# Kernel optimization log

Measured on AMD Instinct MI355X. Metric: run time of the kernel, lower is better.

## Reference

```python
import jax, jax.numpy as jnp
import numpy as np

# hyperparameters from init_kwargs
TEMP = 0.05
MOMENTUM = 0.2
ALPHA = 0.9
TEMP_DIST = 0.6
LAMBDA1 = 1.0
LAMBDA2 = 1.0
EPS_CONS = 2.0
NUM_SAMPLES = 8192
NUM_FEATURES = 2048
B = 256
K = 20
EPS = 1e-12


def setup_inputs() -> dict:
    key = jax.random.key(0)
    ks = jax.random.split(key, 8)
    inputs0 = jax.random.normal(ks[0], (B, NUM_FEATURES), dtype=jnp.float32)
    logits0 = jax.random.normal(ks[1], (B, NUM_SAMPLES), dtype=jnp.float32)
    logits1 = jax.random.normal(ks[2], (B, NUM_SAMPLES), dtype=jnp.float32)
    targets = jax.random.randint(ks[3], (B,), 0, NUM_SAMPLES, dtype=jnp.int32)
    indexes = jnp.arange(B, dtype=jnp.int32)  # global idx == batch idx (identity idx2bidx)
    neighbors = jax.random.randint(ks[4], (B, K), 0, B, dtype=jnp.int32)
    neighbor_dists = jax.random.uniform(ks[5], (B, K), dtype=jnp.float32)
    rampup = jnp.ones((), dtype=jnp.float32)
    features = jax.random.normal(ks[6], (NUM_SAMPLES, NUM_FEATURES), dtype=jnp.float32)
    features = features / jnp.linalg.norm(features, axis=1, keepdims=True)
    return {
        'inputs0': inputs0, 'logits0': logits0, 'logits1': logits1,
        'targets': targets, 'indexes': indexes, 'neighbors': neighbors,
        'neighbor_dists': neighbor_dists, 'rampup': rampup, 'features': features,
    }


def reference(inputs0, logits0, logits1, targets, indexes, neighbors,
              neighbor_dists, rampup, features):
    # F.normalize(inputs[0], dim=1)
    x = inputs0 / jnp.maximum(jnp.linalg.norm(inputs0, axis=1, keepdims=True), EPS)

    # CM forward: scores against memory bank, scaled by temperature
    outputs = (x @ features.T) / TEMP                      # [B, S]
    logp = jax.nn.log_softmax(outputs, axis=-1)
    loss_nce = -jnp.mean(jnp.take_along_axis(logp, targets[:, None], axis=1))

    targets_onehot = jax.nn.one_hot(targets, NUM_SAMPLES, dtype=logits0.dtype)

    # neighbor gathering: indexes = arange(B) so idx2bidx is identity; every
    # neighbor in [0,B) passes the `nb in indexes` filter.
    p0 = jax.nn.softmax(logits0, axis=-1)[neighbors]       # [B, K, S]
    p1 = jax.nn.softmax(logits1, axis=-1)[neighbors]       # [B, K, S]
    # loop appends logits0-row then logits1-row per neighbor -> interleave
    p = jnp.stack([p0, p1], axis=2).reshape(B, 2 * K, NUM_SAMPLES)
    d2 = jnp.repeat(neighbor_dists, 2, axis=1)             # [B, 2K] (d,d pairs)
    w = jax.nn.softmax(d2 / TEMP_DIST, axis=1)             # [B, 2K]
    logits_neighbors1 = jnp.einsum('bk,bks->bs', w, p)     # [B, S]

    # KL branch: neighbors with dist <= eps_consistency (all, since eps=2.0)
    mask = (neighbor_dists <= EPS_CONS).astype(p0.dtype)   # [B, K]
    cnt = jnp.maximum(mask.sum(axis=1, keepdims=True), 1.0)
    logits_neighbors1_KL = jnp.einsum('bk,bks->bs', mask, p0) / cnt  # [B, S]

    refined = ALPHA * targets_onehot + (1.0 - ALPHA) * jax.lax.stop_gradient(logits_neighbors1)
    loss_ce = jnp.mean(jnp.sum(-refined * jax.nn.log_softmax(logits0, axis=-1), axis=1))

    # KLDivLoss(logsoftmax(logits1).detach(), target) with batchmean reduction
    lp1 = jax.lax.stop_gradient(jax.nn.log_softmax(logits1, axis=-1))
    t = logits_neighbors1_KL
    kl = jnp.sum(jnp.where(t > 0, t * (jnp.log(jnp.maximum(t, EPS)) - lp1), 0.0)) / B

    # CM momentum memory-bank scatter update (backward side-effect in torch);
    # equivalent to the sequential loop when targets are unique in the batch.
    upd = MOMENTUM * features[targets] + (1.0 - MOMENTUM) * x
    upd = upd / jnp.maximum(jnp.linalg.norm(upd, axis=1, keepdims=True), EPS)
    new_features = features.at[targets].set(upd)

    return (loss_nce, LAMBDA1 * loss_ce, LAMBDA2 * rampup * kl, new_features)
```

## Files before the change

kernel.cpp:

```cpp
#include <hip/hip_runtime.h>
#include <cmath>

#define NB 256
#define NS 8192
#define NF 2048
#define NK 20

typedef _Float16 half8 __attribute__((ext_vector_type(8)));
typedef _Float16 half4 __attribute__((ext_vector_type(4)));
typedef float f32x4 __attribute__((ext_vector_type(4)));

__device__ __forceinline__ void async16(const void* g, void* l) {
  __builtin_amdgcn_global_load_lds(
      (const __attribute__((address_space(1))) unsigned int*)g,
      (__attribute__((address_space(3))) unsigned int*)l, 16, 0, 0);
}

__device__ __forceinline__ float waveSum(float v) {
#pragma unroll
  for (int off = 32; off > 0; off >>= 1) v += __shfl_xor(v, off, 64);
  return v;
}
__device__ __forceinline__ float waveMax(float v) {
#pragma unroll
  for (int off = 32; off > 0; off >>= 1) v = fmaxf(v, __shfl_xor(v, off, 64));
  return v;
}

__global__ __launch_bounds__(256, 1) void prep(
    const float4* __restrict__ f4, const float* __restrict__ in0,
    const float* __restrict__ logits0, const float* __restrict__ logits1,
    const int* __restrict__ targets, const int* __restrict__ neighbors,
    const float* __restrict__ ndist,
    float* __restrict__ outF, _Float16* __restrict__ fh,
    _Float16* __restrict__ Pt, _Float16* __restrict__ xh,
    _Float16* __restrict__ alpha_h, float* __restrict__ mll,
    _Float16* __restrict__ Wp, float* __restrict__ loss) {
  __shared__ alignas(16) union {
    struct {
      float redA[4];
      float redB[4];
      unsigned long long wmask[4];
    } s;
    _Float16 Lt[16 * 520];
  } sm;
  int tid = threadIdx.x, blk = blockIdx.x;
  int wave = tid >> 6, lane = tid & 63;

  if (blk < NS) {
    int row = blk;
    const float4* fr = f4 + (size_t)row * (NF / 4);
    float4 v0 = fr[tid], v1 = fr[tid + 256];
    half4 h0, h1;
    h0[0] = (_Float16)v0.x; h0[1] = (_Float16)v0.y; h0[2] = (_Float16)v0.z; h0[3] = (_Float16)v0.w;
    h1[0] = (_Float16)v1.x; h1[1] = (_Float16)v1.y; h1[2] = (_Float16)v1.z; h1[3] = (_Float16)v1.w;
    ((half4*)(fh + (size_t)row * NF))[tid] = h0;
    ((half4*)(fh + (size_t)row * NF))[tid + 256] = h1;
    unsigned long long mk = __ballot(targets[tid] == row);
    if (lane == 0) sm.s.wmask[wave] = mk;
    __syncthreads();
    int u = -1;
#pragma unroll
    for (int w = 3; w >= 0; --w)
      if (u < 0 && sm.s.wmask[w])
        u = w * 64 + 63 - (int)__clzll(sm.s.wmask[w]);
    if (u >= 0) {
      const float4* xr = (const float4*)(in0 + (size_t)u * NF);
      float4 a0 = xr[tid], a1 = xr[tid + 256];
      float ssx = a0.x * a0.x + a0.y * a0.y + a0.z * a0.z + a0.w * a0.w +
                  a1.x * a1.x + a1.y * a1.y + a1.z * a1.z + a1.w * a1.w;
      float w1 = waveSum(ssx);
      if (lane == 0) sm.s.redA[wave] = w1;
      __syncthreads();
      float totx = (sm.s.redA[0] + sm.s.redA[1]) + (sm.s.redA[2] + sm.s.redA[3]);
      float ix = 0.8f / fmaxf(sqrtf(totx), 1e-12f);
      v0 = make_float4(0.2f * v0.x + ix * a0.x, 0.2f * v0.y + ix * a0.y,
                       0.2f * v0.z + ix * a0.z, 0.2f * v0.w + ix * a0.w);
      v1 = make_float4(0.2f * v1.x + ix * a1.x, 0.2f * v1.y + ix * a1.y,
                       0.2f * v1.z + ix * a1.z, 0.2f * v1.w + ix * a1.w);
      float ss = v0.x * v0.x + v0.y * v0.y + v0.z * v0.z + v0.w * v0.w +
                 v1.x * v1.x + v1.y * v1.y + v1.z * v1.z + v1.w * v1.w;
      float w2 = waveSum(ss);
      if (lane == 0) sm.s.redB[wave] = w2;
      __syncthreads();
      float tot = (sm.s.redB[0] + sm.s.redB[1]) + (sm.s.redB[2] + sm.s.redB[3]);
      float inv = 1.0f / fmaxf(sqrtf(tot), 1e-12f);
      v0.x *= inv; v0.y *= inv; v0.z *= inv; v0.w *= inv;
      v1.x *= inv; v1.y *= inv; v1.z *= inv; v1.w *= inv;
    }
    float4* o4 = (float4*)(outF + (size_t)row * NF);
    o4[tid] = v0;
    o4[tid + 256] = v1;
  } else if (blk < NS + 512) {
    int r = blk - NS;
    const float* src = (r < NB) ? logits0 : logits1;
    const float4* row = (const float4*)(src + (size_t)(r & (NB - 1)) * NS);
    float4 v[8];
    float mx = -1e30f;
#pragma unroll
    for (int i = 0; i < 8; ++i) {
      v[i] = row[tid + i * 256];
      mx = fmaxf(mx, fmaxf(fmaxf(v[i].x, v[i].y), fmaxf(v[i].z, v[i].w)));
    }
    float wv = waveMax(mx);
    if (lane == 0) sm.s.redA[wave] = wv;
    __syncthreads();
    float m = fmaxf(fmaxf(sm.s.redA[0], sm.s.redA[1]), fmaxf(sm.s.redA[2], sm.s.redA[3]));
    float se = 0.0f;
#pragma unroll
    for (int i = 0; i < 8; ++i)
      se += expf(v[i].x - m) + expf(v[i].y - m) + expf(v[i].z - m) + expf(v[i].w - m);
    float sw = waveSum(se);
    if (lane == 0) sm.s.redB[wave] = sw;
    __syncthreads();
    float l = (sm.s.redB[0] + sm.s.redB[1]) + (sm.s.redB[2] + sm.s.redB[3]);
    if (tid == 0) {
      mll[r] = m + logf(l);
      alpha_h[r] = (_Float16)(256.0f * expf(-m) / l);
    }
  } else if (blk < NS + 1024) {
    int s0 = (blk - (NS + 512)) * 16;
#pragma unroll
    for (int g = 0; g < 8; ++g) {
      int pos = g * 256 + tid;
      int row = pos >> 2, c4 = pos & 3;
      const float* src = ((row < NB) ? logits0 + (size_t)row * NS
                                     : logits1 + (size_t)(row - NB) * NS) + s0 + c4 * 4;
      float4 v = *(const float4*)src;
      sm.Lt[(c4 * 4 + 0) * 520 + row] = (_Float16)expf(v.x);
      sm.Lt[(c4 * 4 + 1) * 520 + row] = (_Float16)expf(v.y);
      sm.Lt[(c4 * 4 + 2) * 520 + row] = (_Float16)expf(v.z);
      sm.Lt[(c4 * 4 + 3) * 520 + row] = (_Float16)expf(v.w);
    }
    __syncthreads();
    int srow = tid >> 4, seg = tid & 15;
    _Float16* dst = Pt + (size_t)(s0 + srow) * 512 + seg * 32;
    const _Float16* lsrc = &sm.Lt[srow * 520 + seg * 32];
#pragma unroll
    for (int q = 0; q < 4; ++q)
      *(half8*)(dst + q * 8) = *(const half8*)(lsrc + q * 8);
  } else if (blk < NS + 1280) {
    int b = blk - (NS + 1024);
    const float4* row = (const float4*)(in0 + (size_t)b * NF);
    float4 v0 = row[tid], v1 = row[tid + 256];
    float ss = v0.x * v0.x + v0.y * v0.y + v0.z * v0.z + v0.w * v0.w +
               v1.x * v1.x + v1.y * v1.y + v1.z * v1.z + v1.w * v1.w;
    float w = waveSum(ss);
    if (lane == 0) sm.s.redA[wave] = w;
    __syncthreads();
    float tot = (sm.s.redA[0] + sm.s.redA[1]) + (sm.s.redA[2] + sm.s.redA[3]);
    float inv = 1.0f / fmaxf(sqrtf(tot), 1e-12f);
    half4 h0, h1;
    h0[0] = (_Float16)(v0.x * inv); h0[1] = (_Float16)(v0.y * inv);
    h0[2] = (_Float16)(v0.z * inv); h0[3] = (_Float16)(v0.w * inv);
    h1[0] = (_Float16)(v1.x * inv); h1[1] = (_Float16)(v1.y * inv);
    h1[2] = (_Float16)(v1.z * inv); h1[3] = (_Float16)(v1.w * inv);
    ((half4*)(xh + (size_t)b * NF))[tid] = h0;
    ((half4*)(xh + (size_t)b * NF))[tid + 256] = h1;
  } else {
    if (tid < 3) loss[tid] = 0.0f;
    float4* W4 = (float4*)Wp;
    for (int i = tid; i < 512 * 512 * 2 / 16; i += 256) W4[i] = make_float4(0, 0, 0, 0);
    __syncthreads();
    int b = tid;
    float d[NK], e[NK];
    int n[NK];
    float s = 0.0f;
    int cnt = 0;
#pragma unroll
    for (int k = 0; k < NK; ++k) {
      d[k] = ndist[b * NK + k];
      n[k] = neighbors[b * NK + k];
      e[k] = expf(d[k] * (1.0f / 0.6f));
      s += e[k];
      cnt += (d[k] <= 2.0f) ? 1 : 0;
    }
    float invs = 1.0f / (2.0f * s);
    float invc = 1.0f / fmaxf((float)cnt, 1.0f);
    _Float16* rkl = Wp + (size_t)b * 512;
    _Float16* rce = Wp + (size_t)(256 + b) * 512;
#pragma unroll
    for (int k = 0; k < NK; ++k) {
      bool first = true;
#pragma unroll
      for (int k2 = 0; k2 < NK; ++k2)
        if (k2 < k && n[k2] == n[k]) first = false;
      if (first) {
        float wsum = 0.0f, ksum = 0.0f;
#pragma unroll
        for (int k2 = 0; k2 < NK; ++k2)
          if (k2 >= k && n[k2] == n[k]) {
            wsum += e[k2] * invs;
            ksum += (d[k2] <= 2.0f) ? invc : 0.0f;
          }
        rkl[n[k]] = (_Float16)ksum;
        rce[n[k]] = (_Float16)wsum;
        rce[256 + n[k]] = (_Float16)wsum;
      }
    }
  }
}

__global__ __launch_bounds__(256) void gemms(
    const _Float16* __restrict__ xh, const _Float16* __restrict__ fh,
    const _Float16* __restrict__ Wp, const _Float16* __restrict__ Pt,
    const _Float16* __restrict__ alpha_h,
    const float* __restrict__ logits0, const float* __restrict__ logits1,
    const float* __restrict__ mll, const int* __restrict__ targets,
    float* __restrict__ pm, float* __restrict__ pl, float* __restrict__ tgt,
    float* __restrict__ part) {
  __shared__ alignas(16) _Float16 As[128 * 64];
  __shared__ alignas(16) _Float16 Bs[128 * 64];
  __shared__ alignas(16) _Float16 Al[512];
  __shared__ float red[4];
  int tid = threadIdx.x, wave = tid >> 6, lane = tid & 63;
  int quad = lane >> 4, r16 = lane & 15, lrow = lane >> 3, lch = lane & 7;
  int blk = blockIdx.x;
  if (blk < 256) {
    int bx = blk & 127, by = blk >> 7;
    int n0 = bx * 64, m0 = by * 128;
    f32x4 acc[2][4] = {};
    for (int k0 = 0; k0 < NF; k0 += 64) {
      __syncthreads();
#pragma unroll
      for (int ss = 0; ss < 4; ++ss) {
        int rl = ss * 32 + wave * 8 + lrow;
        int sc = lch ^ (rl & 7);
        async16(xh + (size_t)(m0 + rl) * NF + k0 + sc * 8, &As[rl * 64 + lch * 8]);
      }
#pragma unroll
      for (int ss = 0; ss < 2; ++ss) {
        int rl = ss * 32 + wave * 8 + lrow;
        int sc = lch ^ (rl & 7);
        async16(fh + (size_t)(n0 + rl) * NF + k0 + sc * 8, &Bs[rl * 64 + lch * 8]);
      }
      __syncthreads();
#pragma unroll
      for (int sub = 0; sub < 2; ++sub) {
        int slot = ((sub * 4 + quad) ^ (r16 & 7)) * 8;
        half8 af[2], bf[4];
#pragma unroll
        for (int i = 0; i < 2; ++i)
          af[i] = *(const half8*)&As[(wave * 32 + i * 16 + r16) * 64 + slot];
#pragma unroll
        for (int j = 0; j < 4; ++j)
          bf[j] = *(const half8*)&Bs[(j * 16 + r16) * 64 + slot];
#pragma unroll
        for (int i = 0; i < 2; ++i)
#pragma unroll
          for (int j = 0; j < 4; ++j)
            acc[i][j] = __builtin_amdgcn_mfma_f32_16x16x32_f16(af[i], bf[j], acc[i][j], 0, 0, 0);
      }
    }
#pragma unroll
    for (int i = 0; i < 2; ++i)
#pragma unroll
      for (int r = 0; r < 4; ++r) {
        int R = m0 + wave * 32 + i * 16 + quad * 4 + r;
        float sv[4];
#pragma unroll
        for (int j = 0; j < 4; ++j) sv[j] = acc[i][j][r] * 20.0f;
        float mx = fmaxf(fmaxf(sv[0], sv[1]), fmaxf(sv[2], sv[3]));
#pragma unroll
        for (int m2 = 1; m2 < 16; m2 <<= 1) mx = fmaxf(mx, __shfl_xor(mx, m2, 64));
        float e = expf(sv[0] - mx) + expf(sv[1] - mx) + expf(sv[2] - mx) + expf(sv[3] - mx);
#pragma unroll
        for (int m2 = 1; m2 < 16; m2 <<= 1) e += __shfl_xor(e, m2, 64);
        int tg = targets[R];
#pragma unroll
        for (int j = 0; j < 4; ++j)
          if (n0 + j * 16 + r16 == tg) tgt[R] = sv[j];
        if (r16 == 0) { pm[R * 128 + bx] = mx; pl[R * 128 + bx] = e; }
      }
  } else {
    int nb = blk - 256;
    int bx = nb & 63, by = nb >> 6;
    int n0 = bx * 128, m0 = by * 128;
    int wm = (wave >> 1) * 64, wn = (wave & 1) * 64;
    if (tid < 64) ((half8*)Al)[tid] = ((const half8*)alpha_h)[tid];
    f32x4 acc[4][4] = {};
    for (int k0 = 0; k0 < 512; k0 += 64) {
      __syncthreads();
#pragma unroll
      for (int ss = 0; ss < 4; ++ss) {
        int rl = ss * 32 + wave * 8 + lrow;
        int sc = lch ^ (rl & 7);
        async16(Wp + (size_t)(m0 + rl) * 512 + k0 + sc * 8, &As[rl * 64 + lch * 8]);
        async16(Pt + (size_t)(n0 + rl) * 512 + k0 + sc * 8, &Bs[rl * 64 + lch * 8]);
      }
      __syncthreads();
#pragma unroll
      for (int sub = 0; sub < 2; ++sub) {
        int slot = ((sub * 4 + quad) ^ (r16 & 7)) * 8;
        half8 alv = *(const half8*)&Al[k0 + slot];
        half8 af[4], bf[4];
#pragma unroll
        for (int i = 0; i < 4; ++i)
          af[i] = *(const half8*)&As[(wm + i * 16 + r16) * 64 + slot];
#pragma unroll
        for (int j = 0; j < 4; ++j)
          bf[j] = *(const half8*)&Bs[(wn + j * 16 + r16) * 64 + slot] * alv;
#pragma unroll
        for (int i = 0; i < 4; ++i)
#pragma unroll
          for (int j = 0; j < 4; ++j)
            acc[i][j] = __builtin_amdgcn_mfma_f32_16x16x32_f16(af[i], bf[j], acc[i][j], 0, 0, 0);
      }
    }
    bool iskl = (by < 2);
    const float* lgbase = iskl ? logits1 : logits0;
    float local = 0.0f;
#pragma unroll
    for (int i = 0; i < 4; ++i)
#pragma unroll
      for (int r = 0; r < 4; ++r) {
        int Mg = m0 + wm + i * 16 + quad * 4 + r;
        int b = iskl ? Mg : (Mg - 256);
        float mv = mll[iskl ? 256 + b : b];
        const float* lgrow = lgbase + (size_t)b * NS + n0 + wn;
#pragma unroll
        for (int j = 0; j < 4; ++j) {
          float lg = lgrow[j * 16 + r16];
          float t = acc[i][j][r] * (1.0f / 256.0f);
          if (iskl)
            local += (t > 0.0f) ? t * (logf(fmaxf(t, 1e-12f)) - (lg - mv)) : 0.0f;
          else
            local += -0.1f * t * (lg - mv);
        }
      }
    float wsv = waveSum(local);
    if (lane == 0) red[wave] = wsv;
    __syncthreads();
    if (tid == 0) part[nb] = (red[0] + red[1]) + (red[2] + red[3]);
  }
}

__global__ __launch_bounds__(128) void final_reduce(
    const float* __restrict__ pm, const float* __restrict__ pl,
    const float* __restrict__ tgt, const float* __restrict__ part,
    const float* __restrict__ logits0, const float* __restrict__ mll,
    const int* __restrict__ targets, const float* __restrict__ rampup,
    float* __restrict__ out) {
  __shared__ float rmx[2], rsm[2];
  int tid = threadIdx.x;
  int b = blockIdx.x;
  float m = pm[b * 128 + tid];
  float l = pl[b * 128 + tid];
  float wm = waveMax(m);
  if ((tid & 63) == 0) rmx[tid >> 6] = wm;
  __syncthreads();
  float mx = fmaxf(rmx[0], rmx[1]);
  float e = l * expf(m - mx);
  float ws = waveSum(e);
  if ((tid & 63) == 0) rsm[tid >> 6] = ws;
  __syncthreads();
  if (tid == 0) {
    float S = rsm[0] + rsm[1];
    float nce = -(tgt[b] - mx - logf(S));
    int tg = targets[b];
    float oh = -0.9f * (logits0[(size_t)b * NS + tg] - mll[b]);
    float pb = part[b];
    float v1 = oh;
    if (b >= 128) v1 += pb;
    atomicAdd(out + 0, nce * (1.0f / 256.0f));
    atomicAdd(out + 1, v1 * (1.0f / 256.0f));
    if (b < 128) atomicAdd(out + 2, rampup[0] * pb * (1.0f / 256.0f));
  }
}

extern "C" void kernel_launch(void* const* d_in, const int* in_sizes, int n_in,
                              void* d_out, int out_size, void* d_ws, size_t ws_size,
                              hipStream_t stream) {
  const float* inputs0 = (const float*)d_in[0];
  const float* logits0 = (const float*)d_in[1];
  const float* logits1 = (const float*)d_in[2];
  const int* targets = (const int*)d_in[3];
  const int* neighbors = (const int*)d_in[5];
  const float* ndist = (const float*)d_in[6];
  const float* rampup = (const float*)d_in[7];
  const float* features = (const float*)d_in[8];
  float* out = (float*)d_out;

  char* ws = (char*)d_ws;
  float* mll = (float*)(ws + 4096);
  _Float16* alpha_h = (_Float16*)(ws + 8192);
  float* part = (float*)(ws + 12288);
  float* tgt = (float*)(ws + 16384);
  float* pm = (float*)(ws + 65536);
  float* pl = (float*)(ws + 196608);
  _Float16* Wp = (_Float16*)(ws + 524288);
  _Float16* xh = (_Float16*)(ws + (3 << 20));
  _Float16* Pt = (_Float16*)(ws + (4 << 20));
  _Float16* fh = (_Float16*)(ws + (12 << 20));

  prep<<<NS + 1281, 256, 0, stream>>>((const float4*)features, inputs0, logits0,
                                      logits1, targets, neighbors, ndist,
                                      out + 3, fh, Pt, xh, alpha_h, mll, Wp, out);
  gemms<<<512, 256, 0, stream>>>(xh, fh, Wp, Pt, alpha_h, logits0, logits1, mll,
                                 targets, pm, pl, tgt, part);
  final_reduce<<<256, 128, 0, stream>>>(pm, pl, tgt, part, logits0, mll, targets,
                                        rampup, out);
}
```

Measured before the change: 211.4 us.

## Fuse feature fp16 conversion and bank copy into GEMM B-tile loads

Removes the 8192-block prep pass that converted the feature bank to fp16 and wrote the copied bank. The GEMM now loads fp32 feature tiles, converts them to fp16 into swizzled LDS itself, and the by==0 blocks write the fp32 copy to the output. The momentum scatter update moves to extra blocks in final_reduce, with the last occurrence of a duplicate target winning. This drops one full read and write pass over the bank and the fp16 intermediate, but the GEMM now loads fp32 tiles synchronously and the fp32-to-fp16 conversion is repeated by both M-row blocks.

```diff
diff --git a/kernel.cpp b/kernel.cpp
--- a/kernel.cpp
+++ b/kernel.cpp
@@ -28,71 +28,24 @@
 }
 
 __global__ __launch_bounds__(256, 1) void prep(
-    const float4* __restrict__ f4, const float* __restrict__ in0,
-    const float* __restrict__ logits0, const float* __restrict__ logits1,
-    const int* __restrict__ targets, const int* __restrict__ neighbors,
-    const float* __restrict__ ndist,
-    float* __restrict__ outF, _Float16* __restrict__ fh,
-    _Float16* __restrict__ Pt, _Float16* __restrict__ xh,
-    _Float16* __restrict__ alpha_h, float* __restrict__ mll,
-    _Float16* __restrict__ Wp, float* __restrict__ loss) {
+    const float* __restrict__ in0, const float* __restrict__ logits0,
+    const float* __restrict__ logits1, const int* __restrict__ neighbors,
+    const float* __restrict__ ndist, _Float16* __restrict__ Pt,
+    _Float16* __restrict__ xh, _Float16* __restrict__ alpha_h,
+    float* __restrict__ mll, _Float16* __restrict__ Wp,
+    float* __restrict__ loss) {
   __shared__ alignas(16) union {
     struct {
       float redA[4];
       float redB[4];
-      unsigned long long wmask[4];
     } s;
     _Float16 Lt[16 * 520];
   } sm;
   int tid = threadIdx.x, blk = blockIdx.x;
   int wave = tid >> 6, lane = tid & 63;
 
-  if (blk < NS) {
-    int row = blk;
-    const float4* fr = f4 + (size_t)row * (NF / 4);
-    float4 v0 = fr[tid], v1 = fr[tid + 256];
-    half4 h0, h1;
-    h0[0] = (_Float16)v0.x; h0[1] = (_Float16)v0.y; h0[2] = (_Float16)v0.z; h0[3] = (_Float16)v0.w;
-    h1[0] = (_Float16)v1.x; h1[1] = (_Float16)v1.y; h1[2] = (_Float16)v1.z; h1[3] = (_Float16)v1.w;
-    ((half4*)(fh + (size_t)row * NF))[tid] = h0;
-    ((half4*)(fh + (size_t)row * NF))[tid + 256] = h1;
-    unsigned long long mk = __ballot(targets[tid] == row);
-    if (lane == 0) sm.s.wmask[wave] = mk;
-    __syncthreads();
-    int u = -1;
-#pragma unroll
-    for (int w = 3; w >= 0; --w)
-      if (u < 0 && sm.s.wmask[w])
-        u = w * 64 + 63 - (int)__clzll(sm.s.wmask[w]);
-    if (u >= 0) {
-      const float4* xr = (const float4*)(in0 + (size_t)u * NF);
-      float4 a0 = xr[tid], a1 = xr[tid + 256];
-      float ssx = a0.x * a0.x + a0.y * a0.y + a0.z * a0.z + a0.w * a0.w +
-                  a1.x * a1.x + a1.y * a1.y + a1.z * a1.z + a1.w * a1.w;
-      float w1 = waveSum(ssx);
-      if (lane == 0) sm.s.redA[wave] = w1;
-      __syncthreads();
-      float totx = (sm.s.redA[0] + sm.s.redA[1]) + (sm.s.redA[2] + sm.s.redA[3]);
-      float ix = 0.8f / fmaxf(sqrtf(totx), 1e-12f);
-      v0 = make_float4(0.2f * v0.x + ix * a0.x, 0.2f * v0.y + ix * a0.y,
-                       0.2f * v0.z + ix * a0.z, 0.2f * v0.w + ix * a0.w);
-      v1 = make_float4(0.2f * v1.x + ix * a1.x, 0.2f * v1.y + ix * a1.y,
-                       0.2f * v1.z + ix * a1.z, 0.2f * v1.w + ix * a1.w);
-      float ss = v0.x * v0.x + v0.y * v0.y + v0.z * v0.z + v0.w * v0.w +
-                 v1.x * v1.x + v1.y * v1.y + v1.z * v1.z + v1.w * v1.w;
-      float w2 = waveSum(ss);
-      if (lane == 0) sm.s.redB[wave] = w2;
-      __syncthreads();
-      float tot = (sm.s.redB[0] + sm.s.redB[1]) + (sm.s.redB[2] + sm.s.redB[3]);
-      float inv = 1.0f / fmaxf(sqrtf(tot), 1e-12f);
-      v0.x *= inv; v0.y *= inv; v0.z *= inv; v0.w *= inv;
-      v1.x *= inv; v1.y *= inv; v1.z *= inv; v1.w *= inv;
-    }
-    float4* o4 = (float4*)(outF + (size_t)row * NF);
-    o4[tid] = v0;
-    o4[tid + 256] = v1;
-  } else if (blk < NS + 512) {
-    int r = blk - NS;
+  if (blk < 512) {
+    int r = blk;
     const float* src = (r < NB) ? logits0 : logits1;
     const float4* row = (const float4*)(src + (size_t)(r & (NB - 1)) * NS);
     float4 v[8];
@@ -118,8 +71,8 @@
       mll[r] = m + logf(l);
       alpha_h[r] = (_Float16)(256.0f * expf(-m) / l);
     }
-  } else if (blk < NS + 1024) {
-    int s0 = (blk - (NS + 512)) * 16;
+  } else if (blk < 1024) {
+    int s0 = (blk - 512) * 16;
 #pragma unroll
     for (int g = 0; g < 8; ++g) {
       int pos = g * 256 + tid;
@@ -139,8 +92,8 @@
 #pragma unroll
     for (int q = 0; q < 4; ++q)
       *(half8*)(dst + q * 8) = *(const half8*)(lsrc + q * 8);
-  } else if (blk < NS + 1280) {
-    int b = blk - (NS + 1024);
+  } else if (blk < 1280) {
+    int b = blk - 1024;
     const float4* row = (const float4*)(in0 + (size_t)b * NF);
     float4 v0 = row[tid], v1 = row[tid + 256];
     float ss = v0.x * v0.x + v0.y * v0.y + v0.z * v0.z + v0.w * v0.w +
@@ -202,13 +155,13 @@
 }
 
 __global__ __launch_bounds__(256) void gemms(
-    const _Float16* __restrict__ xh, const _Float16* __restrict__ fh,
+    const _Float16* __restrict__ xh, const float* __restrict__ fB,
     const _Float16* __restrict__ Wp, const _Float16* __restrict__ Pt,
     const _Float16* __restrict__ alpha_h,
     const float* __restrict__ logits0, const float* __restrict__ logits1,
     const float* __restrict__ mll, const int* __restrict__ targets,
-    float* __restrict__ pm, float* __restrict__ pl, float* __restrict__ tgt,
-    float* __restrict__ part) {
+    float* __restrict__ outF, float* __restrict__ pm, float* __restrict__ pl,
+    float* __restrict__ tgt, float* __restrict__ part) {
   __shared__ alignas(16) _Float16 As[128 * 64];
   __shared__ alignas(16) _Float16 Bs[128 * 64];
   __shared__ alignas(16) _Float16 Al[512];
@@ -219,8 +172,13 @@
   if (blk < 256) {
     int bx = blk & 127, by = blk >> 7;
     int n0 = bx * 64, m0 = by * 128;
+    int c4 = tid & 15, rbase = tid >> 4;
     f32x4 acc[2][4] = {};
     for (int k0 = 0; k0 < NF; k0 += 64) {
+      float4 bv[4];
+#pragma unroll
+      for (int ss = 0; ss < 4; ++ss)
+        bv[ss] = *(const float4*)(fB + (size_t)(n0 + ss * 16 + rbase) * NF + k0 + c4 * 4);
       __syncthreads();
 #pragma unroll
       for (int ss = 0; ss < 4; ++ss) {
@@ -229,10 +187,15 @@
         async16(xh + (size_t)(m0 + rl) * NF + k0 + sc * 8, &As[rl * 64 + lch * 8]);
       }
 #pragma unroll
-      for (int ss = 0; ss < 2; ++ss) {
-        int rl = ss * 32 + wave * 8 + lrow;
-        int sc = lch ^ (rl & 7);
-        async16(fh + (size_t)(n0 + rl) * NF + k0 + sc * 8, &Bs[rl * 64 + lch * 8]);
+      for (int ss = 0; ss < 4; ++ss) {
+        int row = ss * 16 + rbase;
+        half4 h;
+        h[0] = (_Float16)bv[ss].x; h[1] = (_Float16)bv[ss].y;
+        h[2] = (_Float16)bv[ss].z; h[3] = (_Float16)bv[ss].w;
+        int pc = (((c4 >> 1) ^ (row & 7)) << 3) + ((c4 & 1) << 2);
+        *(half4*)&Bs[row * 64 + pc] = h;
+        if (by == 0)
+          *(float4*)(outF + (size_t)(n0 + row) * NF + k0 + c4 * 4) = bv[ss];
       }
       __syncthreads();
 #pragma unroll
@@ -340,31 +303,75 @@
     const float* __restrict__ tgt, const float* __restrict__ part,
     const float* __restrict__ logits0, const float* __restrict__ mll,
     const int* __restrict__ targets, const float* __restrict__ rampup,
-    float* __restrict__ out) {
-  __shared__ float rmx[2], rsm[2];
-  int tid = threadIdx.x;
-  int b = blockIdx.x;
-  float m = pm[b * 128 + tid];
-  float l = pl[b * 128 + tid];
-  float wm = waveMax(m);
-  if ((tid & 63) == 0) rmx[tid >> 6] = wm;
-  __syncthreads();
-  float mx = fmaxf(rmx[0], rmx[1]);
-  float e = l * expf(m - mx);
-  float ws = waveSum(e);
-  if ((tid & 63) == 0) rsm[tid >> 6] = ws;
-  __syncthreads();
-  if (tid == 0) {
-    float S = rsm[0] + rsm[1];
-    float nce = -(tgt[b] - mx - logf(S));
+    const float* __restrict__ in0, const float* __restrict__ features,
+    float* __restrict__ outF, float* __restrict__ out) {
+  __shared__ float rA[2], rB[2];
+  __shared__ int flag;
+  int tid = threadIdx.x, blk = blockIdx.x;
+  if (blk < 256) {
+    int b = blk;
+    float m = pm[b * 128 + tid];
+    float l = pl[b * 128 + tid];
+    float wm = waveMax(m);
+    if ((tid & 63) == 0) rA[tid >> 6] = wm;
+    __syncthreads();
+    float mx = fmaxf(rA[0], rA[1]);
+    float e = l * expf(m - mx);
+    float ws = waveSum(e);
+    if ((tid & 63) == 0) rB[tid >> 6] = ws;
+    __syncthreads();
+    if (tid == 0) {
+      float S = rB[0] + rB[1];
+      float nce = -(tgt[b] - mx - logf(S));
+      int tg = targets[b];
+      float oh = -0.9f * (logits0[(size_t)b * NS + tg] - mll[b]);
+      float pb = part[b];
+      float v1 = oh;
+      if (b >= 128) v1 += pb;
+      atomicAdd(out + 0, nce * (1.0f / 256.0f));
+      atomicAdd(out + 1, v1 * (1.0f / 256.0f));
+      if (b < 128) atomicAdd(out + 2, rampup[0] * pb * (1.0f / 256.0f));
+    }
+  } else {
+    int b = blk - 256;
     int tg = targets[b];
-    float oh = -0.9f * (logits0[(size_t)b * NS + tg] - mll[b]);
-    float pb = part[b];
-    float v1 = oh;
-    if (b >= 128) v1 += pb;
-    atomicAdd(out + 0, nce * (1.0f / 256.0f));
-    atomicAdd(out + 1, v1 * (1.0f / 256.0f));
-    if (b < 128) atomicAdd(out + 2, rampup[0] * pb * (1.0f / 256.0f));
+    if (tid == 0) flag = 0;
+    __syncthreads();
+    bool later = false;
+    for (int i = b + 1 + tid; i < 256; i += 128) later = later || (targets[i] == tg);
+    if (later) flag = 1;
+    __syncthreads();
+    if (flag) return;
+    const float4* xr = (const float4*)(in0 + (size_t)b * NF);
+    const float4* fr = (const float4*)(features + (size_t)tg * NF);
+    float4 a[4];
+    float ssx = 0.0f;
+#pragma unroll
+    for (int s = 0; s < 4; ++s) {
+      a[s] = xr[tid + s * 128];
+      ssx += a[s].x * a[s].x + a[s].y * a[s].y + a[s].z * a[s].z + a[s].w * a[s].w;
+    }
+    float w1 = waveSum(ssx);
+    if ((tid & 63) == 0) rA[tid >> 6] = w1;
+    __syncthreads();
+    float ix = 0.8f / fmaxf(sqrtf(rA[0] + rA[1]), 1e-12f);
+    float4 v[4];
+    float ss = 0.0f;
+#pragma unroll
+    for (int s = 0; s < 4; ++s) {
+      float4 f = fr[tid + s * 128];
+      v[s] = make_float4(0.2f * f.x + ix * a[s].x, 0.2f * f.y + ix * a[s].y,
+                         0.2f * f.z + ix * a[s].z, 0.2f * f.w + ix * a[s].w);
+      ss += v[s].x * v[s].x + v[s].y * v[s].y + v[s].z * v[s].z + v[s].w * v[s].w;
+    }
+    float w2 = waveSum(ss);
+    if ((tid & 63) == 0) rB[tid >> 6] = w2;
+    __syncthreads();
+    float inv = 1.0f / fmaxf(sqrtf(rB[0] + rB[1]), 1e-12f);
+    float4* o4 = (float4*)(outF + (size_t)tg * NF);
+#pragma unroll
+    for (int s = 0; s < 4; ++s)
+      o4[tid + s * 128] = make_float4(v[s].x * inv, v[s].y * inv, v[s].z * inv, v[s].w * inv);
   }
 }
 
@@ -391,13 +398,11 @@
   _Float16* Wp = (_Float16*)(ws + 524288);
   _Float16* xh = (_Float16*)(ws + (3 << 20));
   _Float16* Pt = (_Float16*)(ws + (4 << 20));
-  _Float16* fh = (_Float16*)(ws + (12 << 20));
-
-  prep<<<NS + 1281, 256, 0, stream>>>((const float4*)features, inputs0, logits0,
-                                      logits1, targets, neighbors, ndist,
-                                      out + 3, fh, Pt, xh, alpha_h, mll, Wp, out);
-  gemms<<<512, 256, 0, stream>>>(xh, fh, Wp, Pt, alpha_h, logits0, logits1, mll,
-                                 targets, pm, pl, tgt, part);
-  final_reduce<<<256, 128, 0, stream>>>(pm, pl, tgt, part, logits0, mll, targets,
-                                        rampup, out);
-}
+
+  prep<<<1281, 256, 0, stream>>>(inputs0, logits0, logits1, neighbors, ndist,
+                                 Pt, xh, alpha_h, mll, Wp, out);
+  gemms<<<512, 256, 0, stream>>>(xh, features, Wp, Pt, alpha_h, logits0, logits1,
+                                 mll, targets, out + 3, pm, pl, tgt, part);
+  final_reduce<<<512, 128, 0, stream>>>(pm, pl, tgt, part, logits0, mll, targets,
+                                        rampup, inputs0, features, out + 3, out);
+}
```

Measured after the change: 209.9 us. Within noise of the previous version (-0.7%).
